# Kernel optimization log

Measured on AMD Instinct MI355X. Metric: run time of the kernel, lower is better.

The kernel has to match this reference:

```python
import jax, jax.numpy as jnp
import numpy as np

BS, CH, H, W = 4, 64, 32, 88
N_Z = 60
BEV_Z, BEV_X, BEV_Y = 10, 128, 128  # from round((ranges[i+3]-ranges[i])/voxel_size[i])


def setup_inputs() -> dict:
    key = jax.random.key(0)
    k1, k2, k3, k4 = jax.random.split(key, 4)
    x = jax.random.normal(k1, (BS, CH, H, W), dtype=jnp.float32)
    shp = (BS, N_Z, H, W)
    # integer voxel coords, slightly out of range so the kept-mask drops some points
    xi = jax.random.randint(k2, shp, -2, BEV_X + 2)
    yi = jax.random.randint(k3, shp, -2, BEV_Y + 2)
    zi = jax.random.randint(k4, shp, -1, BEV_Z + 1)
    frustum_xyz = jnp.stack([xi, yi, zi], axis=-1).astype(jnp.int32)  # [B,n_z,H,W,3]
    return {"x": x, "frustum_xyz": frustum_xyz}


def reference(x, frustum_xyz):
    # x: [bs, ch, h, w] camera features; frustum_xyz: [bs, n_z, h, w, 3] voxel coords (x, y, z)
    bs, ch, h, w = x.shape
    nz = frustum_xyz.shape[1]
    # permute(0,2,3,1).unsqueeze(1).expand(bs, nz, h, w, ch)
    feats = jnp.broadcast_to(x.transpose(0, 2, 3, 1)[:, None], (bs, nz, h, w, ch)).reshape(-1, ch)
    f = frustum_xyz.reshape(-1, 3)
    xx, yy, zz = f[:, 0], f[:, 1], f[:, 2]
    b = jnp.repeat(jnp.arange(bs, dtype=f.dtype), nz * h * w)  # batch_idx blocks
    kept = ((xx >= 0) & (xx < BEV_X) & (yy >= 0) & (yy < BEV_Y)
            & (zz >= 0) & (zz < BEV_Z))
    # linear voxel index into dense [bs, Z, X, Y]; invalid points go to a dummy segment.
    # sort + cumsum-trick + unique-scatter in the original == per-voxel segment sum.
    nvox = bs * BEV_Z * BEV_X * BEV_Y
    vox = ((b * BEV_Z + zz) * BEV_X + xx) * BEV_Y + yy
    vox = jnp.where(kept, vox, nvox)
    grid = jax.ops.segment_sum(feats, vox, num_segments=nvox + 1)[:-1]  # drop dummy
    grid = grid.reshape(bs, BEV_Z, BEV_X, BEV_Y, ch)
    # final[b, :, z, x, y] = pooled feats; then .sum(-1) over y -> [bs, ch, Z, X]
    return grid.sum(axis=3).transpose(0, 3, 1, 2)
```

## Files before the change

kernel.cpp:

```cpp
#include <hip/hip_runtime.h>
#include <hip/hip_bf16.h>

#define BS    4
#define CH    64
#define HH    32
#define WW    88
#define NZ    60
#define BEV_Z 10
#define BEV_X 128
#define BEV_Y 128

static constexpr int HW        = HH * WW;
static constexpr int ZX        = BEV_Z * BEV_X;
static constexpr int PTS_PER_B = NZ * HW;

static constexpr int T            = 16;
static constexpr int NT           = HW / T;
static constexpr int CNT_BLOCKS   = BS * NT;
static constexpr int NXELEM       = BS * CH * HW;
static constexpr int XCONV_BLOCKS = NXELEM / 4096;
static constexpr int CNT_WORDS    = ZX * T / 4;
static constexpr int TILE_BYTES   = ZX * T;
static constexpr int ZGROUPS      = ZX / 64;

static constexpr int KS     = 11;
static constexpr int KCH    = HW / KS;
static constexpr int OUTSZ  = BS * CH * ZX;

typedef __attribute__((ext_vector_type(8))) short short8;
typedef __attribute__((ext_vector_type(4))) float floatx4;

__device__ inline unsigned short f2b(float v) {
    __hip_bfloat16 h = __float2bfloat16(v);
    return *reinterpret_cast<unsigned short*>(&h);
}

__device__ inline short cnt2bf(unsigned int w, int s) {
    float fv = (float)((w >> s) & 255u);
    unsigned int u;
    __builtin_memcpy(&u, &fv, 4);
    return (short)(u >> 16);
}

__global__ __launch_bounds__(256)
void build_kernel(const float* __restrict__ x, const int* __restrict__ f,
                  unsigned int* __restrict__ cnt8,
                  unsigned short* __restrict__ xbf) {
    __shared__ unsigned int cnt[CNT_WORDS];
    int blk = blockIdx.x;
    if (blk < CNT_BLOCKS) {
        int b   = blk / NT;
        int t   = blk % NT;
        int hw0 = t * T;
        for (int i = threadIdx.x; i < CNT_WORDS; i += 256) cnt[i] = 0u;
        __syncthreads();

        int hw_l = threadIdx.x & 15;
        int z0   = threadIdx.x >> 4;
        for (int z = z0; z < NZ; z += 16) {
            int p  = b * PTS_PER_B + z * HW + hw0 + hw_l;
            int xx = f[3 * p + 0];
            int yy = f[3 * p + 1];
            int zz = f[3 * p + 2];
            bool kept = (xx >= 0) & (xx < BEV_X) & (yy >= 0) & (yy < BEV_Y) &
                        (zz >= 0) & (zz < BEV_Z);
            if (kept) {
                int cell = (zz * BEV_X + xx) * T + hw_l;
                atomicAdd(&cnt[cell >> 2], 1u << (8 * (cell & 3)));
            }
        }
        __syncthreads();

        unsigned int* obase = cnt8 + (size_t)(b * NT + t) * CNT_WORDS;
        for (int i = threadIdx.x; i < CNT_WORDS; i += 256) obase[i] = cnt[i];
    } else {
        size_t base = (size_t)(blk - CNT_BLOCKS) * 4096;
        #pragma unroll
        for (int r = 0; r < 4; ++r) {
            size_t i = base + ((size_t)r * 256 + threadIdx.x) * 4;
            floatx4 v = *(const floatx4*)(x + i);
            ushort4 o;
            o.x = f2b(v.x); o.y = f2b(v.y); o.z = f2b(v.z); o.w = f2b(v.w);
            *(ushort4*)(xbf + i) = o;
        }
    }
}

__global__ __launch_bounds__(256)
void gemm_kernel(const unsigned short* __restrict__ xbf,
                 const unsigned char* __restrict__ cnt8,
                 float* __restrict__ P) {
    int blk  = blockIdx.x;
    int kc   = blk % KS;
    int r2   = blk / KS;
    int b    = r2 / ZGROUPS;
    int zg   = r2 % ZGROUPS;
    int wave = threadIdx.x >> 6;
    int lane = threadIdx.x & 63;
    int m    = lane & 15;
    int quad = lane >> 4;
    int zx   = zg * 64 + wave * 16 + m;
    int k0   = kc * KCH;

    const unsigned char* pb = cnt8 + (size_t)b * NT * TILE_BYTES
                            + (size_t)(k0 / T + (quad >> 1)) * TILE_BYTES
                            + zx * T + (quad & 1) * 8;
    const unsigned short* pa = xbf + ((size_t)(b * CH) + m) * HW + k0 + quad * 8;

    floatx4 acc0 = {0.f,0.f,0.f,0.f}, acc1 = {0.f,0.f,0.f,0.f};
    floatx4 acc2 = {0.f,0.f,0.f,0.f}, acc3 = {0.f,0.f,0.f,0.f};

    #pragma unroll 2
    for (int kk = 0; kk < KCH; kk += 32) {
        uint2 wv = *(const uint2*)pb;
        pb += 2 * TILE_BYTES;
        short8 bf;
        bf[0] = cnt2bf(wv.x,  0); bf[1] = cnt2bf(wv.x,  8);
        bf[2] = cnt2bf(wv.x, 16); bf[3] = cnt2bf(wv.x, 24);
        bf[4] = cnt2bf(wv.y,  0); bf[5] = cnt2bf(wv.y,  8);
        bf[6] = cnt2bf(wv.y, 16); bf[7] = cnt2bf(wv.y, 24);

        short8 a0 = *(const short8*)(pa + 0 * 16 * HW + kk);
        short8 a1 = *(const short8*)(pa + 1 * 16 * HW + kk);
        short8 a2 = *(const short8*)(pa + 2 * 16 * HW + kk);
        short8 a3 = *(const short8*)(pa + 3 * 16 * HW + kk);

        acc0 = __builtin_amdgcn_mfma_f32_16x16x32_bf16(a0, bf, acc0, 0, 0, 0);
        acc1 = __builtin_amdgcn_mfma_f32_16x16x32_bf16(a1, bf, acc1, 0, 0, 0);
        acc2 = __builtin_amdgcn_mfma_f32_16x16x32_bf16(a2, bf, acc2, 0, 0, 0);
        acc3 = __builtin_amdgcn_mfma_f32_16x16x32_bf16(a3, bf, acc3, 0, 0, 0);
    }

    float* op = P + ((size_t)(kc * BS + b) * CH) * ZX + zx;
    #pragma unroll
    for (int r = 0; r < 4; ++r) {
        int ch = quad * 4 + r;
        op[(0 * 16 + ch) * ZX] = acc0[r];
        op[(1 * 16 + ch) * ZX] = acc1[r];
        op[(2 * 16 + ch) * ZX] = acc2[r];
        op[(3 * 16 + ch) * ZX] = acc3[r];
    }
}

__global__ __launch_bounds__(256)
void reduce_kernel(const float* __restrict__ P, float* __restrict__ out) {
    int idx = blockIdx.x * 256 + threadIdx.x;
    float s = 0.f;
    #pragma unroll
    for (int kc = 0; kc < KS; ++kc)
        s += P[(size_t)kc * OUTSZ + idx];
    out[idx] = s;
}

extern "C" void kernel_launch(void* const* d_in, const int* in_sizes, int n_in,
                              void* d_out, int out_size, void* d_ws, size_t ws_size,
                              hipStream_t stream) {
    const float* x = (const float*)d_in[0];
    const int*   f = (const int*)d_in[1];
    float*       out = (float*)d_out;

    char* ws = (char*)d_ws;
    size_t off = 0;
    auto carve = [&](size_t bytes) {
        char* p = ws + off;
        off += (bytes + 255) & ~(size_t)255;
        return p;
    };
    unsigned int*   cnt8 = (unsigned int*)  carve((size_t)BS * NT * TILE_BYTES);
    unsigned short* xbf  = (unsigned short*)carve((size_t)NXELEM * 2);
    float*          P    = (float*)         carve((size_t)KS * OUTSZ * 4);

    build_kernel <<<CNT_BLOCKS + XCONV_BLOCKS, 256, 0, stream>>>(x, f, cnt8, xbf);
    gemm_kernel  <<<BS * ZGROUPS * KS, 256, 0, stream>>>(xbf, (const unsigned char*)cnt8, P);
    reduce_kernel<<<OUTSZ / 256, 256, 0, stream>>>(P, out);
}
```

Measured before the change: 90.75 us.

## Stage frustum coords in LDS, store bf16 partials, unroll GEMM loop deeper

The count-build phase now loads each block's frustum coordinate slab into shared memory with 16-byte vector loads before doing the atomics, replacing strided scalar global loads. The GEMM writes its split-K partial sums as bf16 instead of fp32, halving the partial buffer traffic, and the reduce kernel unpacks two bf16 values per 32-bit word. The GEMM inner loop is unrolled 4 instead of 2. Storing partials in bf16 loses precision in the output sums, and the extra shared slab raises LDS use in build_kernel.

```diff
diff --git a/kernel.cpp b/kernel.cpp
--- a/kernel.cpp
+++ b/kernel.cpp
@@ -27,6 +27,9 @@
 static constexpr int KCH    = HW / KS;
 static constexpr int OUTSZ  = BS * CH * ZX;
 
+static constexpr int BPTS   = NZ * T;
+static constexpr int FSLAB4 = BPTS * 3 / 4;
+
 typedef __attribute__((ext_vector_type(8))) short short8;
 typedef __attribute__((ext_vector_type(4))) float floatx4;
 
@@ -42,31 +45,49 @@
     return (short)(u >> 16);
 }
 
+__device__ inline float bfbits2f(unsigned int bits) {
+    float fv;
+    __builtin_memcpy(&fv, &bits, 4);
+    return fv;
+}
+
 __global__ __launch_bounds__(256)
 void build_kernel(const float* __restrict__ x, const int* __restrict__ f,
                   unsigned int* __restrict__ cnt8,
                   unsigned short* __restrict__ xbf) {
     __shared__ unsigned int cnt[CNT_WORDS];
+    __shared__ uint4 fslab[FSLAB4];
     int blk = blockIdx.x;
     if (blk < CNT_BLOCKS) {
         int b   = blk / NT;
         int t   = blk % NT;
         int hw0 = t * T;
         for (int i = threadIdx.x; i < CNT_WORDS; i += 256) cnt[i] = 0u;
+
+        int p0 = b * PTS_PER_B + hw0;
+        const uint4* fb = (const uint4*)(f + (size_t)p0 * 3);
+        constexpr int SEG4 = HW * 3 / 4;
+        for (int i = threadIdx.x; i < FSLAB4; i += 256) {
+            int z = i / 12, w16 = i % 12;
+            fslab[i] = fb[(size_t)z * SEG4 + w16];
+        }
         __syncthreads();
 
-        int hw_l = threadIdx.x & 15;
-        int z0   = threadIdx.x >> 4;
-        for (int z = z0; z < NZ; z += 16) {
-            int p  = b * PTS_PER_B + z * HW + hw0 + hw_l;
-            int xx = f[3 * p + 0];
-            int yy = f[3 * p + 1];
-            int zz = f[3 * p + 2];
-            bool kept = (xx >= 0) & (xx < BEV_X) & (yy >= 0) & (yy < BEV_Y) &
-                        (zz >= 0) & (zz < BEV_Z);
-            if (kept) {
-                int cell = (zz * BEV_X + xx) * T + hw_l;
-                atomicAdd(&cnt[cell >> 2], 1u << (8 * (cell & 3)));
+        const unsigned int* fs = (const unsigned int*)fslab;
+        #pragma unroll
+        for (int r = 0; r < 4; ++r) {
+            int j = r * 256 + threadIdx.x;
+            if (j < BPTS) {
+                int xx = (int)fs[j * 3 + 0];
+                int yy = (int)fs[j * 3 + 1];
+                int zz = (int)fs[j * 3 + 2];
+                bool kept = (xx >= 0) & (xx < BEV_X) & (yy >= 0) & (yy < BEV_Y) &
+                            (zz >= 0) & (zz < BEV_Z);
+                if (kept) {
+                    int hw_l = j & 15;
+                    int cell = (zz * BEV_X + xx) * T + hw_l;
+                    atomicAdd(&cnt[cell >> 2], 1u << (8 * (cell & 3)));
+                }
             }
         }
         __syncthreads();
@@ -89,7 +110,7 @@
 __global__ __launch_bounds__(256)
 void gemm_kernel(const unsigned short* __restrict__ xbf,
                  const unsigned char* __restrict__ cnt8,
-                 float* __restrict__ P) {
+                 unsigned short* __restrict__ P) {
     int blk  = blockIdx.x;
     int kc   = blk % KS;
     int r2   = blk / KS;
@@ -110,7 +131,7 @@
     floatx4 acc0 = {0.f,0.f,0.f,0.f}, acc1 = {0.f,0.f,0.f,0.f};
     floatx4 acc2 = {0.f,0.f,0.f,0.f}, acc3 = {0.f,0.f,0.f,0.f};
 
-    #pragma unroll 2
+    #pragma unroll 4
     for (int kk = 0; kk < KCH; kk += 32) {
         uint2 wv = *(const uint2*)pb;
         pb += 2 * TILE_BYTES;
@@ -131,25 +152,28 @@
         acc3 = __builtin_amdgcn_mfma_f32_16x16x32_bf16(a3, bf, acc3, 0, 0, 0);
     }
 
-    float* op = P + ((size_t)(kc * BS + b) * CH) * ZX + zx;
+    unsigned short* op = P + ((size_t)(kc * BS + b) * CH) * ZX + zx;
     #pragma unroll
     for (int r = 0; r < 4; ++r) {
         int ch = quad * 4 + r;
-        op[(0 * 16 + ch) * ZX] = acc0[r];
-        op[(1 * 16 + ch) * ZX] = acc1[r];
-        op[(2 * 16 + ch) * ZX] = acc2[r];
-        op[(3 * 16 + ch) * ZX] = acc3[r];
+        op[(0 * 16 + ch) * ZX] = f2b(acc0[r]);
+        op[(1 * 16 + ch) * ZX] = f2b(acc1[r]);
+        op[(2 * 16 + ch) * ZX] = f2b(acc2[r]);
+        op[(3 * 16 + ch) * ZX] = f2b(acc3[r]);
     }
 }
 
 __global__ __launch_bounds__(256)
-void reduce_kernel(const float* __restrict__ P, float* __restrict__ out) {
+void reduce_kernel(const unsigned int* __restrict__ P, float* __restrict__ out) {
     int idx = blockIdx.x * 256 + threadIdx.x;
-    float s = 0.f;
+    float s_lo = 0.f, s_hi = 0.f;
     #pragma unroll
-    for (int kc = 0; kc < KS; ++kc)
-        s += P[(size_t)kc * OUTSZ + idx];
-    out[idx] = s;
+    for (int kc = 0; kc < KS; ++kc) {
+        unsigned int u = P[(size_t)kc * (OUTSZ / 2) + idx];
+        s_lo += bfbits2f(u << 16);
+        s_hi += bfbits2f(u & 0xFFFF0000u);
+    }
+    *(float2*)(out + (size_t)idx * 2) = make_float2(s_lo, s_hi);
 }
 
 extern "C" void kernel_launch(void* const* d_in, const int* in_sizes, int n_in,
@@ -168,9 +192,9 @@
     };
     unsigned int*   cnt8 = (unsigned int*)  carve((size_t)BS * NT * TILE_BYTES);
     unsigned short* xbf  = (unsigned short*)carve((size_t)NXELEM * 2);
-    float*          P    = (float*)         carve((size_t)KS * OUTSZ * 4);
+    unsigned short* P    = (unsigned short*)carve((size_t)KS * OUTSZ * 2);
 
     build_kernel <<<CNT_BLOCKS + XCONV_BLOCKS, 256, 0, stream>>>(x, f, cnt8, xbf);
     gemm_kernel  <<<BS * ZGROUPS * KS, 256, 0, stream>>>(xbf, (const unsigned char*)cnt8, P);
-    reduce_kernel<<<OUTSZ / 256, 256, 0, stream>>>(P, out);
-}
+    reduce_kernel<<<OUTSZ / 2 / 256, 256, 0, stream>>>((const unsigned int*)P, out);
+}
```

Measured after the change: 88.10 us. 2.9% less time.
